# Performance work log

Measured on AMD Instinct MI355X. Metric: run time of the kernel, lower is better.

Reference implementation:

```python
import jax, jax.numpy as jnp
import numpy as np

NUM_HEADS = 8
HEAD_DIM = 64
D_MODEL = NUM_HEADS * HEAD_DIM  # 512
B, T = 4, 2048


def setup_inputs() -> dict:
    key = jax.random.key(0)
    k1, k2 = jax.random.split(key)
    x = jax.random.normal(k1, (B, T, D_MODEL), dtype=jnp.float32)
    mask = jnp.ones((B, 1, T, T), dtype=jnp.float32)
    W = jax.random.normal(k2, (D_MODEL, 3 * D_MODEL), dtype=jnp.float32) * (D_MODEL ** -0.5)
    b = jnp.zeros((3 * D_MODEL,), dtype=jnp.float32)
    return {"x": x, "mask": mask, "W": W, "b": b}


def reference(x, mask, W, b):
    batch = x.shape[0]
    # fused QKV projection: [B, T, 3D]
    qkv = jnp.einsum("btd,de->bte", x, W) + b
    # NOTE: faithful to torch reshape [B, T, H, Hd, 3] -> the size-3 axis is innermost
    qkv = qkv.reshape(batch, -1, NUM_HEADS, HEAD_DIM, 3)
    qkv = jnp.transpose(qkv, (4, 0, 2, 1, 3))  # [3, B, H, T, Hd]
    q, k, v = qkv[0], qkv[1], qkv[2]
    logits = jnp.einsum("bhqd,bhkd->bhqk", q, k) / (HEAD_DIM ** 0.5)
    logits = logits + (1.0 - mask) * -10000.0
    w = jax.nn.softmax(logits, axis=-1)
    out = jnp.einsum("bhqk,bhkd->bhqd", w, v)  # [B, H, T, Hd]
    out = jnp.transpose(out, (0, 2, 1, 3)).reshape(batch, -1, NUM_HEADS * HEAD_DIM)
    return out
```

## Files before the change

kernel.cpp:

```cpp
#include <hip/hip_runtime.h>
#include <hip/hip_bf16.h>
#include <stdint.h>

#define B_   4
#define T_   2048
#define H_   8
#define HD_  64
#define DM_  512
#define N3_  1536

typedef short bf_el;
typedef __attribute__((ext_vector_type(8))) bf_el bfrag;
typedef __attribute__((ext_vector_type(4))) float ffrag;

#define SCALE_L2E  0.18033688011112043f
#define MASK_L2E   14426.950408889634f

static __device__ __forceinline__ unsigned short f2bf(float f) {
    union { float f; unsigned int i; } v; v.f = f;
    unsigned int r = v.i + 0x7fff + ((v.i >> 16) & 1);
    return (unsigned short)(r >> 16);
}
static __device__ __forceinline__ unsigned short f2bf_fast(float f) {
    union { float f; unsigned int i; } v; v.f = f;
    return (unsigned short)((v.i + 0x8000u) >> 16);
}

__global__ __launch_bounds__(256) void k_prep(const float* __restrict__ W,
                                              const float* __restrict__ X,
                                              const float* __restrict__ mask,
                                              unsigned short* __restrict__ Wt,
                                              unsigned short* __restrict__ Xb,
                                              int* __restrict__ flags) {
    __shared__ __align__(16) unsigned short Ls[64 * 72];
    const int bid = blockIdx.x;
    const int tid = threadIdx.x;

    if (bid < 512) {
        const int R0 = bid * 16;
        const int mb = R0 >> 11;
        const int q0 = R0 & 2047;
        const int e  = mb * 32 + (q0 >> 6);
        const int wave = tid >> 6, lane = tid & 63;
        unsigned int acc = 0u;
        const float* base = mask + (size_t)R0 * T_ + tid * 8;
#pragma unroll
        for (int rr = 0; rr < 16; ++rr) {
            const uint4 u0 = *(const uint4*)(base + (size_t)rr * T_);
            const uint4 u1 = *(const uint4*)(base + (size_t)rr * T_ + 4);
            acc |= (u0.x ^ 0x3F800000u) | (u0.y ^ 0x3F800000u) |
                   (u0.z ^ 0x3F800000u) | (u0.w ^ 0x3F800000u) |
                   (u1.x ^ 0x3F800000u) | (u1.y ^ 0x3F800000u) |
                   (u1.z ^ 0x3F800000u) | (u1.w ^ 0x3F800000u);
        }
        unsigned long long bal = __ballot(acc != 0u);
        if (lane == 0 && bal != 0ULL) {
#pragma unroll
            for (int j = 0; j < 8; ++j)
                if ((bal >> (8 * j)) & 0xFFULL)
                    atomicOr(&flags[e * 32 + wave * 8 + j], 1);
        }
        return;
    }
    if (bid < 768) {
        const int b2 = bid - 512;
        const float* src = X + (size_t)b2 * 16384;
        unsigned short* dst = Xb + (size_t)b2 * 16384;
#pragma unroll
        for (int j = 0; j < 8; ++j) {
            int idx = j * 512 + tid * 2;
            float4 f0 = *(const float4*)(src + idx * 4);
            float4 f1 = *(const float4*)(src + idx * 4 + 4);
            __align__(16) unsigned short t8[8];
            t8[0] = f2bf_fast(f0.x); t8[1] = f2bf_fast(f0.y);
            t8[2] = f2bf_fast(f0.z); t8[3] = f2bf_fast(f0.w);
            t8[4] = f2bf_fast(f1.x); t8[5] = f2bf_fast(f1.y);
            t8[6] = f2bf_fast(f1.z); t8[7] = f2bf_fast(f1.w);
            *(uint4*)(dst + idx * 4) = *(const uint4*)t8;
        }
        return;
    }
    {
        const int t  = bid - 768;
        const int n0 = (t % 24) * 64;
        const int k0 = (t / 24) * 64;
#pragma unroll
        for (int i = 0; i < 4; ++i) {
            int chunk = tid + i * 256;
            int k = chunk >> 4;
            int c = chunk & 15;
            float4 f = *(const float4*)(W + (size_t)(k0 + k) * N3_ + n0 + c * 4);
            unsigned short* p = Ls + k * 72 + c * 4;
            p[0] = f2bf(f.x); p[1] = f2bf(f.y); p[2] = f2bf(f.z); p[3] = f2bf(f.w);
        }
        __syncthreads();
        const int n = tid >> 2;
        const int g = tid & 3;
        __align__(16) unsigned short tmp[16];
#pragma unroll
        for (int i = 0; i < 16; ++i) tmp[i] = Ls[(g * 16 + i) * 72 + n];
        uint4* dst = (uint4*)(Wt + (size_t)(n0 + n) * DM_ + k0 + g * 16);
        dst[0] = *(const uint4*)(tmp);
        dst[1] = *(const uint4*)(tmp + 8);
    }
}

__global__ __launch_bounds__(256, 4) void k_gemm_qkv(const unsigned short* __restrict__ Xb,
                                                     const unsigned short* __restrict__ Wt,
                                                     const float* __restrict__ bias,
                                                     unsigned short* __restrict__ Qb,
                                                     unsigned short* __restrict__ Kb,
                                                     unsigned short* __restrict__ Vtb) {
    __shared__ __align__(16) unsigned short SH[12800];
    unsigned short* As = SH;
    unsigned short* Bs = SH + 2560;
    unsigned short* Cs = SH;

    const int tid  = threadIdx.x;
    const int wave = tid >> 6;
    const int lane = tid & 63;
    const int quad = lane >> 4;
    const int l16  = lane & 15;
    const int wm = wave >> 1, wn = wave & 1;
    const int h  = blockIdx.x >> 7;
    const int m0 = (blockIdx.x & 127) * 64;
    const int n0 = h * 192;

    float bvv[6];
#pragma unroll
    for (int ni = 0; ni < 6; ++ni) bvv[ni] = bias[n0 + wn * 96 + ni * 16 + l16];

    ffrag acc[2][6];
#pragma unroll
    for (int i = 0; i < 2; ++i)
#pragma unroll
        for (int j = 0; j < 6; ++j) acc[i][j] = (ffrag){0.f, 0.f, 0.f, 0.f};

    const int ar = tid >> 2, ac = tid & 3;
    const int br0 = tid >> 2, br1 = (tid + 256) >> 2, br2 = (tid + 512) >> 2;
    const int bc  = tid & 3;
    uint4 pa, pb0, pb1, pb2;

    pa  = *(const uint4*)(Xb + (size_t)(m0 + ar) * DM_ + ac * 8);
    pb0 = *(const uint4*)(Wt + (size_t)(n0 + br0) * DM_ + bc * 8);
    pb1 = *(const uint4*)(Wt + (size_t)(n0 + br1) * DM_ + bc * 8);
    pb2 = *(const uint4*)(Wt + (size_t)(n0 + br2) * DM_ + bc * 8);

    for (int kt = 0; kt < 16; ++kt) {
        __syncthreads();
        *(uint4*)(As + ar * 40 + ac * 8)  = pa;
        *(uint4*)(Bs + br0 * 40 + bc * 8) = pb0;
        *(uint4*)(Bs + br1 * 40 + bc * 8) = pb1;
        *(uint4*)(Bs + br2 * 40 + bc * 8) = pb2;
        __syncthreads();
        if (kt < 15) {
            const int ko = (kt + 1) * 32;
            pa  = *(const uint4*)(Xb + (size_t)(m0 + ar) * DM_ + ko + ac * 8);
            pb0 = *(const uint4*)(Wt + (size_t)(n0 + br0) * DM_ + ko + bc * 8);
            pb1 = *(const uint4*)(Wt + (size_t)(n0 + br1) * DM_ + ko + bc * 8);
            pb2 = *(const uint4*)(Wt + (size_t)(n0 + br2) * DM_ + ko + bc * 8);
        }
        bfrag af[2], bfr[6];
#pragma unroll
        for (int mi = 0; mi < 2; ++mi)
            af[mi] = *(const bfrag*)(As + (wm * 32 + mi * 16 + l16) * 40 + quad * 8);
#pragma unroll
        for (int ni = 0; ni < 6; ++ni)
            bfr[ni] = *(const bfrag*)(Bs + (wn * 96 + ni * 16 + l16) * 40 + quad * 8);
#pragma unroll
        for (int mi = 0; mi < 2; ++mi)
#pragma unroll
            for (int ni = 0; ni < 6; ++ni)
                acc[mi][ni] = __builtin_amdgcn_mfma_f32_16x16x32_bf16(af[mi], bfr[ni], acc[mi][ni], 0, 0, 0);
    }

    const int b  = m0 >> 11;
    const int tb = m0 & 2047;
    const size_t bh = (size_t)(b * 8 + h);
    float cscale[6];
#pragma unroll
    for (int ni = 0; ni < 6; ++ni) {
        int c = wn * 96 + ni * 16 + l16;
        cscale[ni] = (c % 3 == 0) ? SCALE_L2E : 1.0f;
    }
    __syncthreads();
#pragma unroll
    for (int mi = 0; mi < 2; ++mi)
#pragma unroll
        for (int ni = 0; ni < 6; ++ni)
#pragma unroll
            for (int reg = 0; reg < 4; ++reg) {
                int r = wm * 32 + mi * 16 + quad * 4 + reg;
                int c = wn * 96 + ni * 16 + l16;
                Cs[r * 200 + c] = f2bf_fast((acc[mi][ni][reg] + bvv[ni]) * cscale[ni]);
            }
    __syncthreads();
#pragma unroll
    for (int i = 0; i < 2; ++i) {
        int idx = tid + i * 256;
        int tl = idx >> 3, hc = (idx & 7) * 8;
        __align__(16) unsigned short tq[8], tk[8];
#pragma unroll
        for (int j = 0; j < 8; ++j) {
            tq[j] = Cs[tl * 200 + (hc + j) * 3 + 0];
            tk[j] = Cs[tl * 200 + (hc + j) * 3 + 1];
        }
        *(uint4*)(Qb + (bh * T_ + tb + tl) * HD_ + hc) = *(const uint4*)tq;
        *(uint4*)(Kb + (bh * T_ + tb + tl) * HD_ + hc) = *(const uint4*)tk;
    }
#pragma unroll
    for (int i = 0; i < 2; ++i) {
        int idx = tid + i * 256;
        int hd = idx >> 3, t8 = (idx & 7) * 8;
        __align__(16) unsigned short tv[8];
#pragma unroll
        for (int j = 0; j < 8; ++j)
            tv[j] = Cs[(t8 + j) * 200 + hd * 3 + 2];
        *(uint4*)(Vtb + (bh * HD_ + hd) * T_ + tb + t8) = *(const uint4*)tv;
    }
}

__global__ __launch_bounds__(256) void k_attn(const unsigned short* __restrict__ Q,
                                              const unsigned short* __restrict__ K,
                                              const unsigned short* __restrict__ Vt,
                                              const float* __restrict__ mask,
                                              const int* __restrict__ flags,
                                              float* __restrict__ out) {
    __shared__ __align__(16) unsigned short Ks[64 * 72];
    __shared__ __align__(16) unsigned short Vs[64 * 72];
    __shared__ __align__(16) unsigned short Ps[4][16 * 72];

    const int tid = threadIdx.x;
    const int wave = tid >> 6, lane = tid & 63;
    const int quad = lane >> 4, l16 = lane & 15;
    const int bh = blockIdx.x & 31, b = bh >> 3, h = bh & 7;
    const int qt = blockIdx.x >> 5;
    const int q0 = qt * 64;
    const int fbase = (b * 32 + qt) * 32;

    bfrag qf[2];
    {
        size_t qrow = ((size_t)bh * T_ + q0 + wave * 16 + l16) * HD_;
        qf[0] = *(const bfrag*)(Q + qrow + quad * 8);
        qf[1] = *(const bfrag*)(Q + qrow + 32 + quad * 8);
    }
    float lsum[4] = {0.f, 0.f, 0.f, 0.f};
    ffrag of[4];
#pragma unroll
    for (int nb = 0; nb < 4; ++nb) of[nb] = (ffrag){0.f, 0.f, 0.f, 0.f};

    const int sr0 = tid >> 3, sr1 = (tid + 256) >> 3, sc = tid & 7;
    const unsigned short* Kbase = K  + (size_t)bh * T_ * HD_;
    const unsigned short* Vbase = Vt + (size_t)bh * HD_ * T_;

    for (int kt = 0; kt < 32; ++kt) {
        __syncthreads();
        {
            const int kn = kt * 64;
            *(uint4*)(Ks + sr0 * 72 + sc * 8) =
                *(const uint4*)(Kbase + (size_t)(kn + sr0) * HD_ + sc * 8);
            *(uint4*)(Ks + sr1 * 72 + sc * 8) =
                *(const uint4*)(Kbase + (size_t)(kn + sr1) * HD_ + sc * 8);
            *(uint4*)(Vs + sr0 * 72 + sc * 8) =
                *(const uint4*)(Vbase + (size_t)sr0 * T_ + kn + sc * 8);
            *(uint4*)(Vs + sr1 * 72 + sc * 8) =
                *(const uint4*)(Vbase + (size_t)sr1 * T_ + kn + sc * 8);
        }
        const int fl = flags[fbase + kt];
        __syncthreads();
        ffrag sf[4];
#pragma unroll
        for (int ns = 0; ns < 4; ++ns) {
            ffrag a = (ffrag){0.f, 0.f, 0.f, 0.f};
#pragma unroll
            for (int ks = 0; ks < 2; ++ks) {
                bfrag kf = *(const bfrag*)(Ks + (ns * 16 + l16) * 72 + (ks * 4 + quad) * 8);
                a = __builtin_amdgcn_mfma_f32_16x16x32_bf16(qf[ks], kf, a, 0, 0, 0);
            }
            sf[ns] = a;
        }
        if (fl) {
#pragma unroll
            for (int reg = 0; reg < 4; ++reg) {
                int tq = q0 + wave * 16 + quad * 4 + reg;
                const float* mrow = mask + ((size_t)b * T_ + tq) * T_ + kt * 64;
#pragma unroll
                for (int ns = 0; ns < 4; ++ns) {
                    float msk = mrow[ns * 16 + l16];
                    float p = __builtin_amdgcn_exp2f(
                        fmaf(msk, MASK_L2E, sf[ns][reg] - MASK_L2E));
                    lsum[reg] += p;
                    Ps[wave][(quad * 4 + reg) * 72 + ns * 16 + l16] = f2bf_fast(p);
                }
            }
        } else {
#pragma unroll
            for (int reg = 0; reg < 4; ++reg) {
#pragma unroll
                for (int ns = 0; ns < 4; ++ns) {
                    float p = __builtin_amdgcn_exp2f(sf[ns][reg]);
                    lsum[reg] += p;
                    Ps[wave][(quad * 4 + reg) * 72 + ns * 16 + l16] = f2bf_fast(p);
                }
            }
        }
#pragma unroll
        for (int ks = 0; ks < 2; ++ks) {
            bfrag pf = *(const bfrag*)(&Ps[wave][l16 * 72 + (ks * 4 + quad) * 8]);
#pragma unroll
            for (int nb = 0; nb < 4; ++nb) {
                bfrag vf = *(const bfrag*)(Vs + (nb * 16 + l16) * 72 + (ks * 4 + quad) * 8);
                of[nb] = __builtin_amdgcn_mfma_f32_16x16x32_bf16(pf, vf, of[nb], 0, 0, 0);
            }
        }
    }
#pragma unroll
    for (int reg = 0; reg < 4; ++reg) {
        float s = lsum[reg];
#pragma unroll
        for (int d = 1; d < 16; d <<= 1) s += __shfl_xor(s, d, 64);
        float inv = 1.0f / s;
        int t = q0 + wave * 16 + quad * 4 + reg;
#pragma unroll
        for (int nb = 0; nb < 4; ++nb)
            out[((size_t)b * T_ + t) * DM_ + h * 64 + nb * 16 + l16] = of[nb][reg] * inv;
    }
}

extern "C" void kernel_launch(void* const* d_in, const int* in_sizes, int n_in,
                              void* d_out, int out_size, void* d_ws, size_t ws_size,
                              hipStream_t stream) {
    const float* X    = (const float*)d_in[0];
    const float* mask = (const float*)d_in[1];
    const float* W    = (const float*)d_in[2];
    const float* bias = (const float*)d_in[3];
    float* outp = (float*)d_out;

    char* ws = (char*)d_ws;
    unsigned short* Wt  = (unsigned short*)(ws);
    unsigned short* Xb  = (unsigned short*)(ws + 1572864);
    unsigned short* Qb  = (unsigned short*)(ws + 9961472);
    unsigned short* Kb  = (unsigned short*)(ws + 18350080);
    unsigned short* Vtb = (unsigned short*)(ws + 26738688);
    int*            flg = (int*)(ws + 35127296);

    hipMemsetAsync(flg, 0, 16384, stream);
    k_prep     <<<dim3(960),  256, 0, stream>>>(W, X, mask, Wt, Xb, flg);
    k_gemm_qkv <<<dim3(1024), 256, 0, stream>>>(Xb, Wt, bias, Qb, Kb, Vtb);
    k_attn     <<<dim3(1024), 256, 0, stream>>>(Qb, Kb, Vtb, mask, flg, outp);
}
```

Measured before the change: 224.0 us.

## Compute transposed S so P stays in registers, skipping the LDS round-trip

```diff
diff --git a/kernel.cpp b/kernel.cpp
--- a/kernel.cpp
+++ b/kernel.cpp
@@ -11,6 +11,7 @@
 
 typedef short bf_el;
 typedef __attribute__((ext_vector_type(8))) bf_el bfrag;
+typedef __attribute__((ext_vector_type(4))) bf_el bfrag4;
 typedef __attribute__((ext_vector_type(4))) float ffrag;
 
 #define SCALE_L2E  0.18033688011112043f
@@ -228,7 +229,6 @@
                                               float* __restrict__ out) {
     __shared__ __align__(16) unsigned short Ks[64 * 72];
     __shared__ __align__(16) unsigned short Vs[64 * 72];
-    __shared__ __align__(16) unsigned short Ps[4][16 * 72];
 
     const int tid = threadIdx.x;
     const int wave = tid >> 6, lane = tid & 63;
@@ -237,21 +237,23 @@
     const int qt = blockIdx.x >> 5;
     const int q0 = qt * 64;
     const int fbase = (b * 32 + qt) * 32;
+    const int q = q0 + wave * 16 + l16;
 
     bfrag qf[2];
     {
-        size_t qrow = ((size_t)bh * T_ + q0 + wave * 16 + l16) * HD_;
+        size_t qrow = ((size_t)bh * T_ + q) * HD_;
         qf[0] = *(const bfrag*)(Q + qrow + quad * 8);
         qf[1] = *(const bfrag*)(Q + qrow + 32 + quad * 8);
     }
-    float lsum[4] = {0.f, 0.f, 0.f, 0.f};
+    float lsum = 0.f;
     ffrag of[4];
 #pragma unroll
-    for (int nb = 0; nb < 4; ++nb) of[nb] = (ffrag){0.f, 0.f, 0.f, 0.f};
+    for (int dt = 0; dt < 4; ++dt) of[dt] = (ffrag){0.f, 0.f, 0.f, 0.f};
 
     const int sr0 = tid >> 3, sr1 = (tid + 256) >> 3, sc = tid & 7;
     const unsigned short* Kbase = K  + (size_t)bh * T_ * HD_;
     const unsigned short* Vbase = Vt + (size_t)bh * HD_ * T_;
+    const float* mq = mask + ((size_t)b * T_ + q) * T_;
 
     for (int kt = 0; kt < 32; ++kt) {
         __syncthreads();
@@ -268,62 +270,50 @@
         }
         const int fl = flags[fbase + kt];
         __syncthreads();
-        ffrag sf[4];
 #pragma unroll
         for (int ns = 0; ns < 4; ++ns) {
             ffrag a = (ffrag){0.f, 0.f, 0.f, 0.f};
 #pragma unroll
             for (int ks = 0; ks < 2; ++ks) {
                 bfrag kf = *(const bfrag*)(Ks + (ns * 16 + l16) * 72 + (ks * 4 + quad) * 8);
-                a = __builtin_amdgcn_mfma_f32_16x16x32_bf16(qf[ks], kf, a, 0, 0, 0);
+                a = __builtin_amdgcn_mfma_f32_16x16x32_bf16(kf, qf[ks], a, 0, 0, 0);
             }
-            sf[ns] = a;
-        }
-        if (fl) {
-#pragma unroll
-            for (int reg = 0; reg < 4; ++reg) {
-                int tq = q0 + wave * 16 + quad * 4 + reg;
-                const float* mrow = mask + ((size_t)b * T_ + tq) * T_ + kt * 64;
-#pragma unroll
-                for (int ns = 0; ns < 4; ++ns) {
-                    float msk = mrow[ns * 16 + l16];
+            bfrag4 pf;
+            if (fl) {
+                const float* mp = mq + kt * 64 + ns * 16 + quad * 4;
+#pragma unroll
+                for (int reg = 0; reg < 4; ++reg) {
                     float p = __builtin_amdgcn_exp2f(
-                        fmaf(msk, MASK_L2E, sf[ns][reg] - MASK_L2E));
-                    lsum[reg] += p;
-                    Ps[wave][(quad * 4 + reg) * 72 + ns * 16 + l16] = f2bf_fast(p);
+                        fmaf(mp[reg], MASK_L2E, a[reg] - MASK_L2E));
+                    lsum += p;
+                    pf[reg] = (bf_el)f2bf_fast(p);
+                }
+            } else {
+#pragma unroll
+                for (int reg = 0; reg < 4; ++reg) {
+                    float p = __builtin_amdgcn_exp2f(a[reg]);
+                    lsum += p;
+                    pf[reg] = (bf_el)f2bf_fast(p);
                 }
             }
-        } else {
-#pragma unroll
-            for (int reg = 0; reg < 4; ++reg) {
-#pragma unroll
-                for (int ns = 0; ns < 4; ++ns) {
-                    float p = __builtin_amdgcn_exp2f(sf[ns][reg]);
-                    lsum[reg] += p;
-                    Ps[wave][(quad * 4 + reg) * 72 + ns * 16 + l16] = f2bf_fast(p);
-                }
+#pragma unroll
+            for (int dt = 0; dt < 4; ++dt) {
+                bfrag4 vf = *(const bfrag4*)(Vs + (dt * 16 + l16) * 72 + ns * 16 + quad * 4);
+                of[dt] = __builtin_amdgcn_mfma_f32_16x16x16bf16_1k(vf, pf, of[dt], 0, 0, 0);
             }
         }
-#pragma unroll
-        for (int ks = 0; ks < 2; ++ks) {
-            bfrag pf = *(const bfrag*)(&Ps[wave][l16 * 72 + (ks * 4 + quad) * 8]);
-#pragma unroll
-            for (int nb = 0; nb < 4; ++nb) {
-                bfrag vf = *(const bfrag*)(Vs + (nb * 16 + l16) * 72 + (ks * 4 + quad) * 8);
-                of[nb] = __builtin_amdgcn_mfma_f32_16x16x32_bf16(pf, vf, of[nb], 0, 0, 0);
-            }
-        }
-    }
-#pragma unroll
-    for (int reg = 0; reg < 4; ++reg) {
-        float s = lsum[reg];
-#pragma unroll
-        for (int d = 1; d < 16; d <<= 1) s += __shfl_xor(s, d, 64);
-        float inv = 1.0f / s;
-        int t = q0 + wave * 16 + quad * 4 + reg;
-#pragma unroll
-        for (int nb = 0; nb < 4; ++nb)
-            out[((size_t)b * T_ + t) * DM_ + h * 64 + nb * 16 + l16] = of[nb][reg] * inv;
+    }
+    float s = lsum;
+    s += __shfl_xor(s, 16, 64);
+    s += __shfl_xor(s, 32, 64);
+    const float inv = 1.0f / s;
+    float* orow = out + ((size_t)b * T_ + q) * DM_ + h * 64;
+#pragma unroll
+    for (int dt = 0; dt < 4; ++dt) {
+        float4 v;
+        v.x = of[dt][0] * inv; v.y = of[dt][1] * inv;
+        v.z = of[dt][2] * inv; v.w = of[dt][3] * inv;
+        *(float4*)(orow + dt * 16 + quad * 4) = v;
     }
 }
 
```

Result: no change. 222.8 us (-0.5%).
